# Performance work log

Hardware: AMD Instinct MI355X
Metric: run time of the kernel (lower is better)

## Reference

```python
import jax, jax.numpy as jnp
from jax import lax
import numpy as np

B = 2048; IMG = 28; K = 3; CIN = 1; HC = 32; LC = 16; WID = 64; HID = 64
LIS = IMG - 3 * (K - 1)           # 22: latent image size
FLAT = LIS * LIS * HC             # 15488
BLK = WID * LC                    # 1024: hypernet block size
T1 = 10.0; T0 = 0.0; NSTEP = 20   # fixed-step RK4 replaces adaptive dopri5
VAR = 0.1                         # p_z0 diagonal covariance


def _conv(x, w, b):  # w: [Cout,Cin,k,k], VALID conv, stride 1
    y = lax.conv_general_dilated(x, w, (1, 1), 'VALID',
                                 dimension_numbers=('NCHW', 'OIHW', 'NCHW'))
    return y + b[None, :, None, None]


def _convT(x, w, b):  # w: [Cin,Cout,k,k] (pytorch ConvTranspose2d layout)
    wf = jnp.flip(w, (2, 3)).transpose(1, 0, 2, 3)  # -> OIHW, spatially flipped
    y = lax.conv_general_dilated(x, wf, (1, 1), [(K - 1, K - 1), (K - 1, K - 1)],
                                 dimension_numbers=('NCHW', 'OIHW', 'NCHW'))
    return y + b[None, :, None, None]


def _forward(x, c0w, c0b, c1w, c1b, c2w, c2b, elw, elb, dlw, dlb,
             t0w, t0b, t1w, t1b, t2w, t2b, h1w, h1b, h2w, h2b, h3w, h3b):
    # ---- encoder (dropout in eval = identity) ----
    h = jnp.tanh(_conv(x, c0w, c0b))
    h = jnp.tanh(_conv(h, c1w, c1b))
    h = jnp.tanh(_conv(h, c2w, c2b))
    z1 = h.reshape(h.shape[0], -1) @ elw + elb          # [B, LC]
    # ---- decoder ----
    d = jnp.tanh(z1 @ dlw + dlb)                         # [B, FLAT]
    d = d.reshape(-1, HC, LIS, LIS)
    d = jnp.tanh(_convT(d, t0w, t0b))
    d = jnp.tanh(_convT(d, t1w, t1b))
    recon = _convT(d, t2w, t2b)                          # [B, CIN, 28, 28]

    # ---- CNF vector field with analytic trace ----
    def hyper(t):
        p = jnp.tanh(jnp.reshape(jnp.asarray(t, jnp.float32), (1, 1)) @ h1w + h1b)
        p = jnp.tanh(p @ h2w + h2b)
        p = (p @ h3w + h3b).reshape(-1)
        W = p[:BLK].reshape(WID, LC)
        U = p[BLK:2 * BLK].reshape(WID, LC) * jax.nn.sigmoid(p[2 * BLK:3 * BLK].reshape(WID, LC))
        Bb = p[3 * BLK:]                                 # [WID]
        return W, Bb, U

    def f(t, z):
        W, Bb, U = hyper(t)
        hh = jnp.tanh(jnp.einsum('bd,wd->wb', z, W) + Bb[:, None])   # [WID, B]
        dz = jnp.einsum('wb,wd->bd', hh, U) / WID                     # [B, LC]
        s = jnp.sum(W * U, axis=1)                                    # [WID]: sum_i W_w[i]U_w[i]
        tr = jnp.mean((1.0 - hh * hh) * s[:, None], axis=0)           # [B] analytic trace
        return dz, -tr[:, None]

    dt = (T0 - T1) / NSTEP

    def step(state, i):
        z, lp = state
        t = T1 + i * dt
        k1z, k1l = f(t, z)
        k2z, k2l = f(t + 0.5 * dt, z + 0.5 * dt * k1z)
        k3z, k3l = f(t + 0.5 * dt, z + 0.5 * dt * k2z)
        k4z, k4l = f(t + dt, z + dt * k3z)
        z = z + dt / 6.0 * (k1z + 2 * k2z + 2 * k3z + k4z)
        lp = lp + dt / 6.0 * (k1l + 2 * k2l + 2 * k3l + k4l)
        return (z, lp), None

    lp1 = jnp.zeros((z1.shape[0], 1), z1.dtype)
    (z0, lp0), _ = lax.scan(step, (z1, lp1), jnp.arange(NSTEP, dtype=jnp.float32))

    # MultivariateNormal(0, 0.1*I) log_prob
    logp = -0.5 * (LC * jnp.log(2 * jnp.pi) + LC * jnp.log(VAR) + jnp.sum(z0 * z0, -1) / VAR)
    x_probs = jnp.mean(logp - lp0[:, 0])
    return recon, x_probs


def setup_inputs() -> dict:
    key = jax.random.key(0)
    ks = jax.random.split(key, 16)
    n = jax.random.normal
    s = jnp.float32(0.05)
    z = jnp.zeros
    OUT3 = 3 * BLK + WID
    return {
        'x': n(ks[0], (B, CIN, IMG, IMG), jnp.float32),
        'c0w': n(ks[1], (HC, CIN, K, K)) * s, 'c0b': z((HC,)),
        'c1w': n(ks[2], (HC, HC, K, K)) * s, 'c1b': z((HC,)),
        'c2w': n(ks[3], (HC, HC, K, K)) * s, 'c2b': z((HC,)),
        'elw': n(ks[4], (FLAT, LC)) * s, 'elb': z((LC,)),
        'dlw': n(ks[5], (LC, FLAT)) * s, 'dlb': z((FLAT,)),
        't0w': n(ks[6], (HC, HC, K, K)) * s, 't0b': z((HC,)),
        't1w': n(ks[7], (HC, HC, K, K)) * s, 't1b': z((HC,)),
        't2w': n(ks[8], (HC, CIN, K, K)) * s, 't2b': z((CIN,)),
        'h1w': n(ks[9], (1, HID)) * s, 'h1b': z((HID,)),
        'h2w': n(ks[10], (HID, HID)) * s, 'h2b': z((HID,)),
        'h3w': n(ks[11], (HID, OUT3)) * s, 'h3b': z((OUT3,)),
    }


def reference(x, c0w, c0b, c1w, c1b, c2w, c2b, elw, elb, dlw, dlb,
              t0w, t0b, t1w, t1b, t2w, t2b, h1w, h1b, h2w, h2b, h3w, h3b):
    return _forward(x, c0w, c0b, c1w, c1b, c2w, c2b, elw, elb, dlw, dlb,
                    t0w, t0b, t1w, t1b, t2w, t2b, h1w, h1b, h2w, h2b, h3w, h3b)
```

## Files before the change

kernel.cpp:

```cpp
#include <hip/hip_runtime.h>
#include <math.h>

#define Bsz 2048

using bf16x8 = __attribute__((ext_vector_type(8))) short;
using f32x4  = __attribute__((ext_vector_type(4))) float;

__device__ __forceinline__ float fast_tanh(float x){
    float e = __expf(2.0f * x);
    return 1.0f - 2.0f / (e + 1.0f);
}
__device__ __forceinline__ float fast_sigmoid(float x){
    return 1.0f / (1.0f + __expf(-x));
}
__device__ __forceinline__ unsigned short f2b(float f){
    union { float f; unsigned u; } v; v.f = f;
    unsigned r = v.u + 0x7FFFu + ((v.u >> 16) & 1u);
    return (unsigned short)(r >> 16);
}
__device__ __forceinline__ float b2f(unsigned short s){
    union { unsigned u; float f; } v; v.u = ((unsigned)s) << 16;
    return v.f;
}

__device__ __forceinline__ float stage_t(int sidx){
    int i  = sidx >> 2, st = sidx & 3;
    float t = 10.0f - 0.5f * (float)i;
    if (st == 1 || st == 2) t -= 0.25f;
    else if (st == 3)       t -= 0.5f;
    return t;
}

__global__ void k_prep(const float* __restrict__ c1w, const float* __restrict__ c2w,
                       const float* __restrict__ t0w, const float* __restrict__ t1w,
                       const float* __restrict__ elw, const float* __restrict__ dlw,
                       const float* __restrict__ elb,
                       unsigned short* __restrict__ wc1, unsigned short* __restrict__ wc2,
                       unsigned short* __restrict__ wt0, unsigned short* __restrict__ wt1,
                       unsigned short* __restrict__ elwT, unsigned short* __restrict__ dlwT,
                       float* __restrict__ z1, int full){
    int gsz = gridDim.x * 256;
    for (int i = blockIdx.x*256 + threadIdx.x; i < 9216; i += gsz){
        int ci = i & 31, co = (i >> 5) & 31, s = i >> 10;
        wc1[i] = f2b(c1w[(co*32 + ci)*9 + s]);
        wc2[i] = f2b(c2w[(co*32 + ci)*9 + s]);
        wt0[i] = f2b(t0w[(ci*32 + co)*9 + (8 - s)]);
        wt1[i] = f2b(t1w[(ci*32 + co)*9 + (8 - s)]);
    }
    if (!full) return;
    for (int i = blockIdx.x*256 + threadIdx.x; i < 32768; i += gsz)
        z1[i] = elb[i & 15];
    for (int i = blockIdx.x*256 + threadIdx.x; i < 247808; i += gsz){
        int l = i / 15488, f2 = i - l*15488;
        int pos = f2 >> 5, ci = f2 & 31;
        elwT[i] = f2b(elw[(ci*484 + pos)*16 + l]);
    }
    for (int i = blockIdx.x*256 + threadIdx.x; i < 247808; i += gsz){
        int f2 = i >> 4, l = i & 15;
        int pos = f2 >> 5, ci = f2 & 31;
        dlwT[i] = f2b(dlw[l*15488 + ci*484 + pos]);
    }
}

__global__ void __launch_bounds__(256)
k_conv0(const float* __restrict__ x, const float* __restrict__ c0w,
        const float* __restrict__ c0b, unsigned short* __restrict__ A0,
        int cb, int CH){
    int gid = blockIdx.x*256 + threadIdx.x;
    if (gid >= CH*676) return;
    int b = gid / 676, pos = gid - b*676;
    int y = pos / 26, xx = pos - y*26;
    const float* xin = x + (size_t)(cb + b)*784;
    float v[9];
#pragma unroll
    for (int r = 0; r < 3; r++)
#pragma unroll
        for (int s = 0; s < 3; s++)
            v[r*3+s] = xin[(y+r)*28 + xx + s];
    unsigned short* ob = A0 + (size_t)b*21632 + pos*32;
#pragma unroll
    for (int g = 0; g < 8; g++){
        float a0 = c0b[g*4+0], a1 = c0b[g*4+1], a2 = c0b[g*4+2], a3 = c0b[g*4+3];
#pragma unroll
        for (int k = 0; k < 9; k++){
            a0 += v[k] * c0w[(g*4+0)*9 + k];
            a1 += v[k] * c0w[(g*4+1)*9 + k];
            a2 += v[k] * c0w[(g*4+2)*9 + k];
            a3 += v[k] * c0w[(g*4+3)*9 + k];
        }
        ushort4 o;
        o.x = f2b(fast_tanh(a0)); o.y = f2b(fast_tanh(a1));
        o.z = f2b(fast_tanh(a2)); o.w = f2b(fast_tanh(a3));
        *(ushort4*)(ob + g*4) = o;
    }
}

template<int IL, int OL, int OW, int OOFF, int INS, int OUTS>
__global__ void __launch_bounds__(256)
k_convM(const unsigned short* __restrict__ in, const unsigned short* __restrict__ wg,
        const float* __restrict__ bias, unsigned short* __restrict__ out, int CH){
    constexpr int N  = OL * OL;
    constexpr int NT = (N + 15) / 16;
    const int tid = threadIdx.x;
    const int wave = tid >> 6, lane = tid & 63;
    const int q = lane >> 4, nn = lane & 15;
    const int nw = gridDim.x * 4;

    bf16x8 af[2][9];
#pragma unroll
    for (int mt = 0; mt < 2; mt++)
#pragma unroll
        for (int s = 0; s < 9; s++)
            af[mt][s] = *(const bf16x8*)(wg + s*1024 + (mt*16 + nn)*32 + q*8);
    float4 bc0 = *(const float4*)(bias + q*4);
    float4 bc1 = *(const float4*)(bias + 16 + q*4);

    for (int t = blockIdx.x*4 + wave; t < CH*NT; t += nw){
        int img = t / NT, tt = t - img*NT;
        const unsigned short* inb = in + (size_t)img * INS;
        unsigned short* outb = out + (size_t)img * OUTS;
        int pos = tt*16 + nn;
        int pc  = pos < N ? pos : N - 1;
        int oy = pc / OL, ox = pc - oy*OL;
        const unsigned short* ib = inb + (oy*IL + ox)*32 + q*8;
        f32x4 acc0 = {0.f,0.f,0.f,0.f}, acc1 = {0.f,0.f,0.f,0.f};
#pragma unroll
        for (int r = 0; r < 3; r++){
            bf16x8 b0 = *(const bf16x8*)(ib + (r*IL + 0)*32);
            bf16x8 b1 = *(const bf16x8*)(ib + (r*IL + 1)*32);
            bf16x8 b2 = *(const bf16x8*)(ib + (r*IL + 2)*32);
            acc0 = __builtin_amdgcn_mfma_f32_16x16x32_bf16(af[0][r*3+0], b0, acc0, 0,0,0);
            acc1 = __builtin_amdgcn_mfma_f32_16x16x32_bf16(af[1][r*3+0], b0, acc1, 0,0,0);
            acc0 = __builtin_amdgcn_mfma_f32_16x16x32_bf16(af[0][r*3+1], b1, acc0, 0,0,0);
            acc1 = __builtin_amdgcn_mfma_f32_16x16x32_bf16(af[1][r*3+1], b1, acc1, 0,0,0);
            acc0 = __builtin_amdgcn_mfma_f32_16x16x32_bf16(af[0][r*3+2], b2, acc0, 0,0,0);
            acc1 = __builtin_amdgcn_mfma_f32_16x16x32_bf16(af[1][r*3+2], b2, acc1, 0,0,0);
        }
        if (pos < N){
            int opix = oy*OW + ox + OOFF;
            ushort4 o0, o1;
            o0.x = f2b(fast_tanh(acc0[0] + bc0.x)); o0.y = f2b(fast_tanh(acc0[1] + bc0.y));
            o0.z = f2b(fast_tanh(acc0[2] + bc0.z)); o0.w = f2b(fast_tanh(acc0[3] + bc0.w));
            o1.x = f2b(fast_tanh(acc1[0] + bc1.x)); o1.y = f2b(fast_tanh(acc1[1] + bc1.y));
            o1.z = f2b(fast_tanh(acc1[2] + bc1.z)); o1.w = f2b(fast_tanh(acc1[3] + bc1.w));
            *(ushort4*)(outb + opix*32 + q*4)      = o0;
            *(ushort4*)(outb + opix*32 + 16 + q*4) = o1;
        }
    }
}

__global__ void __launch_bounds__(256)
k_encg(const unsigned short* __restrict__ A2, const unsigned short* __restrict__ elwT,
       float* __restrict__ z1, int cb, int CH){
    int wave = threadIdx.x >> 6, lane = threadIdx.x & 63;
    int q = lane >> 4, nn = lane & 15;
    int imgb = blockIdx.x*16;
    const unsigned short* ap = A2 + (size_t)(imgb + nn)*21632 + q*8;
    const unsigned short* bp = elwT + (size_t)nn*15488 + q*8;
    f32x4 acc = {0.f,0.f,0.f,0.f};
    int s0 = blockIdx.y*121;
#pragma unroll 2
    for (int s = s0 + wave; s < s0 + 121; s += 4){
        bf16x8 a = *(const bf16x8*)(ap + s*32);
        bf16x8 b = *(const bf16x8*)(bp + s*32);
        acc = __builtin_amdgcn_mfma_f32_16x16x32_bf16(a, b, acc, 0,0,0);
    }
    float* zp = z1 + (size_t)(cb + imgb)*16;
#pragma unroll
    for (int i = 0; i < 4; i++)
        atomicAdd(zp + (q*4 + i)*16 + nn, acc[i]);
}

__global__ void __launch_bounds__(256)
k_decg(const float* __restrict__ z1, const unsigned short* __restrict__ dlwT,
       const float* __restrict__ dlb, unsigned short* __restrict__ D0,
       unsigned short* __restrict__ D1, int cb, int CH){
    __shared__ float zl[256];
    int tid = threadIdx.x, ib = blockIdx.y;
    zl[tid] = z1[(size_t)(cb + ib*16 + (tid >> 4))*16 + (tid & 15)];
    __syncthreads();
    if (blockIdx.x >= 61){
        int hid = (blockIdx.x - 61)*256 + tid;
        uint4 zq = {0,0,0,0};
        for (int p = hid; p < 16*676; p += 1280){
            int im = p / 676, px = p - im*676;
            int y = px / 26, x = px - y*26;
            if (y < 2 || y >= 24 || x < 2 || x >= 24){
                uint4* pt = (uint4*)(D0 + (size_t)(ib*16 + im)*21632 + px*32);
                pt[0] = zq; pt[1] = zq; pt[2] = zq; pt[3] = zq;
            }
        }
        for (int p = hid; p < 16*784; p += 1280){
            int im = p / 784, px = p - im*784;
            int y = px / 28, x = px - y*28;
            if (y < 2 || y >= 26 || x < 2 || x >= 26){
                uint4* pt = (uint4*)(D1 + (size_t)(ib*16 + im)*25088 + px*32);
                pt[0] = zq; pt[1] = zq; pt[2] = zq; pt[3] = zq;
            }
        }
        return;
    }
    int ci = tid & 31, po = tid >> 5;
    int pos = blockIdx.x*8 + po;
    if (pos >= 484) return;
    int y = pos / 22, xx = pos - y*22;
    float bias = dlb[ci*484 + pos];
    const unsigned short* w = dlwT + (size_t)(pos*32 + ci)*16;
    bf16x8 w0 = *(const bf16x8*)(w);
    bf16x8 w1 = *(const bf16x8*)(w + 8);
    float wf[16];
#pragma unroll
    for (int j = 0; j < 8; j++){
        wf[j]   = b2f((unsigned short)w0[j]);
        wf[8+j] = b2f((unsigned short)w1[j]);
    }
    int opix = ((y+2)*26 + xx + 2)*32 + ci;
#pragma unroll 1
    for (int i = 0; i < 16; i++){
        float a = bias;
#pragma unroll
        for (int l = 0; l < 16; l++) a += zl[i*16 + l] * wf[l];
        D0[(size_t)(ib*16 + i)*21632 + opix] = f2b(fast_tanh(a));
    }
}

__global__ void __launch_bounds__(256)
k_convT2(const unsigned short* __restrict__ D2, const float* __restrict__ t2w,
         const float* __restrict__ t2b, float* __restrict__ out, int cb, int CH){
    int gid = blockIdx.x*256 + threadIdx.x;
    if (gid >= CH*784) return;
    int b = gid / 784, o = gid - b*784;
    int y = o / 28, xx = o - y*28;
    const unsigned short* db = D2 + (size_t)b*21632;
    float a = t2b[0];
#pragma unroll
    for (int r = 0; r < 3; r++){
        int iy = y + r - 2;
        if ((unsigned)iy >= 26u) continue;
#pragma unroll
        for (int s = 0; s < 3; s++){
            int ix = xx + s - 2;
            if ((unsigned)ix >= 26u) continue;
            const unsigned short* pp = db + (iy*26 + ix)*32;
            int wi = (2-r)*3 + (2-s);
#pragma unroll
            for (int g = 0; g < 4; g++){
                bf16x8 h = *(const bf16x8*)(pp + g*8);
#pragma unroll
                for (int j = 0; j < 8; j++)
                    a += b2f((unsigned short)h[j]) * t2w[(g*8+j)*9 + wi];
            }
        }
    }
    out[(size_t)(cb + b)*784 + o] = a;
}

template<int LOUT, int INW, int OUTW, int OUTOFF>
__device__ __forceinline__ void conv_gemm(const unsigned short* __restrict__ Wg,
                                          const float* __restrict__ bias,
                                          const unsigned short* inL,
                                          unsigned short* outL, int tid){
    constexpr int N  = LOUT * LOUT;
    constexpr int NT = (N + 15) / 16;
    const int lane  = tid & 63;
    const int wave  = tid >> 6;
    const int mtile = wave & 1;
    const int quad  = lane >> 4;
    const int nn    = lane & 15;
    bf16x8 afr[9];
    const unsigned short* wp = Wg + (mtile*16 + nn)*32 + quad*8;
#pragma unroll
    for (int s = 0; s < 9; s++)
        afr[s] = *(const bf16x8*)(wp + s*1024);
    float4 bco = *(const float4*)(bias + mtile*16 + quad*4);
    for (int t = (wave >> 1); t < NT; t += 2){
        int pos = t*16 + nn;
        int pc  = pos < N ? pos : N - 1;
        int y = pc / LOUT, x = pc - y*LOUT;
        const unsigned short* ib = inL + (y*INW + x)*32 + quad*8;
        f32x4 acc = {0.f, 0.f, 0.f, 0.f};
#pragma unroll
        for (int r = 0; r < 3; r++)
#pragma unroll
            for (int s = 0; s < 3; s++)
                acc = __builtin_amdgcn_mfma_f32_16x16x32_bf16(
                        afr[r*3+s], *(const bf16x8*)(ib + (r*INW + s)*32), acc, 0, 0, 0);
        if (pos < N){
            ushort4 o;
            o.x = f2b(fast_tanh(acc[0] + bco.x));
            o.y = f2b(fast_tanh(acc[1] + bco.y));
            o.z = f2b(fast_tanh(acc[2] + bco.z));
            o.w = f2b(fast_tanh(acc[3] + bco.w));
            int opix = y*OUTW + x + OUTOFF;
            *(ushort4*)(outL + opix*32 + mtile*16 + quad*4) = o;
        }
    }
}

__global__ void __launch_bounds__(256)
k_enc_f(const float* __restrict__ x,
        const float* __restrict__ c0w, const float* __restrict__ c0b,
        const unsigned short* __restrict__ wc1, const float* __restrict__ c1b,
        const unsigned short* __restrict__ wc2, const float* __restrict__ c2b,
        const float* __restrict__ elw, const float* __restrict__ elb,
        float* __restrict__ z1){
    __shared__ float X[784];
    __shared__ __align__(16) unsigned short H0[21632];
    __shared__ __align__(16) unsigned short H1[18432];
    __shared__ __align__(16) unsigned short H2[15488];
    __shared__ float red[16*17];
    const int tid = threadIdx.x, b = blockIdx.x;
    for (int i = tid; i < 784; i += 256) X[i] = x[b*784 + i];
    __syncthreads();
    for (int pos = tid; pos < 676; pos += 256){
        int y = pos / 26, xx = pos - y*26;
        float v[9];
#pragma unroll
        for (int r = 0; r < 3; r++)
#pragma unroll
            for (int s = 0; s < 3; s++)
                v[r*3+s] = X[(y+r)*28 + xx + s];
#pragma unroll
        for (int g = 0; g < 8; g++){
            float a0 = c0b[g*4+0], a1 = c0b[g*4+1], a2 = c0b[g*4+2], a3 = c0b[g*4+3];
#pragma unroll
            for (int k = 0; k < 9; k++){
                a0 += v[k] * c0w[(g*4+0)*9 + k];
                a1 += v[k] * c0w[(g*4+1)*9 + k];
                a2 += v[k] * c0w[(g*4+2)*9 + k];
                a3 += v[k] * c0w[(g*4+3)*9 + k];
            }
            ushort4 o;
            o.x = f2b(fast_tanh(a0)); o.y = f2b(fast_tanh(a1));
            o.z = f2b(fast_tanh(a2)); o.w = f2b(fast_tanh(a3));
            *(ushort4*)(H0 + pos*32 + g*4) = o;
        }
    }
    __syncthreads();
    conv_gemm<24, 26, 24, 0>(wc1, c1b, H0, H1, tid);
    __syncthreads();
    conv_gemm<22, 24, 22, 0>(wc2, c2b, H1, H2, tid);
    __syncthreads();
    {
        int fg = tid >> 4, l = tid & 15;
        float a = 0.f;
        for (int ci = 0; ci < 32; ci++)
            for (int pos = fg; pos < 484; pos += 16)
                a += b2f(H2[pos*32 + ci]) * elw[(ci*484 + pos)*16 + l];
        red[fg*17 + l] = a;
        __syncthreads();
        if (tid < 16){
            float s = elb[tid];
#pragma unroll
            for (int g = 0; g < 16; g++) s += red[g*17 + tid];
            z1[b*16 + tid] = s;
        }
    }
}

__global__ void __launch_bounds__(256)
k_dec_f(const float* __restrict__ z1,
        const float* __restrict__ dlw, const float* __restrict__ dlb,
        const unsigned short* __restrict__ wt0, const float* __restrict__ t0b,
        const unsigned short* __restrict__ wt1, const float* __restrict__ t1b,
        const float* __restrict__ t2w, const float* __restrict__ t2b,
        float* __restrict__ out){
    __shared__ __align__(16) unsigned short D0[21632];
    __shared__ __align__(16) unsigned short D1[25088];
    __shared__ __align__(16) unsigned short D2[28800];
    const int tid = threadIdx.x, b = blockIdx.x;
    {
        uint4 zq = {0,0,0,0};
        for (int i = tid; i < 2704; i += 256) ((uint4*)D0)[i] = zq;
        for (int i = tid; i < 3136; i += 256) ((uint4*)D1)[i] = zq;
        for (int i = tid; i < 3600; i += 256) ((uint4*)D2)[i] = zq;
    }
    float zz[16];
#pragma unroll
    for (int l = 0; l < 16; l++) zz[l] = z1[b*16 + l];
    __syncthreads();
    for (int f = tid; f < 15488; f += 256){
        float a = dlb[f];
#pragma unroll
        for (int l = 0; l < 16; l++) a += zz[l] * dlw[l*15488 + f];
        int ci = f / 484, pos = f - ci*484;
        int y = pos / 22, xx = pos - y*22;
        D0[((y+2)*26 + xx + 2)*32 + ci] = f2b(fast_tanh(a));
    }
    __syncthreads();
    conv_gemm<24, 26, 28, 58>(wt0, t0b, D0, D1, tid);
    __syncthreads();
    conv_gemm<26, 28, 30, 62>(wt1, t1b, D1, D2, tid);
    __syncthreads();
    for (int o = tid; o < 784; o += 256){
        int y = o / 28, xx = o - y*28;
        float a = t2b[0];
#pragma unroll
        for (int r = 0; r < 3; r++)
#pragma unroll
            for (int s = 0; s < 3; s++){
                const unsigned short* pp = D2 + ((y+r)*30 + xx + s)*32;
                int wi = (2-r)*3 + (2-s);
#pragma unroll
                for (int g = 0; g < 4; g++){
                    bf16x8 h = *(const bf16x8*)(pp + g*8);
#pragma unroll
                    for (int j = 0; j < 8; j++)
                        a += b2f((unsigned short)h[j]) * t2w[(g*8+j)*9 + wi];
                }
            }
        out[(size_t)b*784 + o] = a;
    }
}

__global__ void __launch_bounds__(64)
k_hyp1(const float* __restrict__ h1w, const float* __restrict__ h1b,
       const float* __restrict__ h2w, const float* __restrict__ h2b,
       float* __restrict__ p2ws){
    __shared__ float p1l[64];
    int sidx = blockIdx.x, tid = threadIdx.x;
    float t = stage_t(sidx);
    p1l[tid] = fast_tanh(t * h1w[tid] + h1b[tid]);
    __syncthreads();
    float a0 = h2b[tid], a1 = 0.f, a2 = 0.f, a3 = 0.f;
#pragma unroll
    for (int k = 0; k < 64; k += 4){
        a0 += p1l[k]   * h2w[(k)*64   + tid];
        a1 += p1l[k+1] * h2w[(k+1)*64 + tid];
        a2 += p1l[k+2] * h2w[(k+2)*64 + tid];
        a3 += p1l[k+3] * h2w[(k+3)*64 + tid];
    }
    p2ws[sidx*64 + tid] = fast_tanh((a0 + a1) + (a2 + a3));
}

__global__ void __launch_bounds__(256)
k_hyp2(const float* __restrict__ p2ws, const float* __restrict__ h3w,
       const float* __restrict__ h3b, float* __restrict__ p3ws){
    __shared__ float p2l[64];
    int sidx = blockIdx.y, tid = threadIdx.x;
    if (tid < 64) p2l[tid] = p2ws[sidx*64 + tid];
    __syncthreads();
    int m = blockIdx.x*256 + tid;
    if (m >= 3136) return;
    const float* hp = h3w + m;
    float a0 = h3b[m], a1 = 0.f, a2 = 0.f, a3 = 0.f;
#pragma unroll
    for (int k = 0; k < 64; k += 4){
        a0 += p2l[k]   * hp[(size_t)(k)*3136];
        a1 += p2l[k+1] * hp[(size_t)(k+1)*3136];
        a2 += p2l[k+2] * hp[(size_t)(k+2)*3136];
        a3 += p2l[k+3] * hp[(size_t)(k+3)*3136];
    }
    p3ws[(size_t)sidx*3200 + m] = (a0 + a1) + (a2 + a3);
}

__global__ void __launch_bounds__(256)
k_hyp3(const float* __restrict__ p3ws, float* __restrict__ hyp){
    __shared__ float sred[64];
    int sidx = blockIdx.x, tid = threadIdx.x;
    const float* p3 = p3ws + (size_t)sidx*3200;
    float* g = hyp + (size_t)sidx*2048;
    unsigned short* gW = (unsigned short*)g;
    unsigned short* gU = (unsigned short*)(g + 1024);

    {
        int lane = tid & 63, c = tid >> 6;
        int q = lane >> 4, m = lane & 15;
        ushort4 o0 = {0,0,0,0}, o1 = {0,0,0,0};
        if (q < 2){
            const float* wp = p3 + (c*16 + m)*16 + q*8;
            o0.x = f2b(wp[0]); o0.y = f2b(wp[1]); o0.z = f2b(wp[2]); o0.w = f2b(wp[3]);
            o1.x = f2b(wp[4]); o1.y = f2b(wp[5]); o1.z = f2b(wp[6]); o1.w = f2b(wp[7]);
        }
        *(ushort4*)(gW + tid*8)     = o0;
        *(ushort4*)(gW + tid*8 + 4) = o1;
    }
    if (tid < 128){
        int lane = tid & 63, kb = tid >> 6;
        int q = lane >> 4, d = lane & 15;
        unsigned short uo[8];
#pragma unroll
        for (int j = 0; j < 8; j++){
            int w = kb*32 + q*8 + j;
            float u = p3[1024 + w*16 + d] * fast_sigmoid(p3[2048 + w*16 + d]);
            uo[j] = f2b(u);
        }
        *(ushort4*)(gU + tid*8)     = *(ushort4*)&uo[0];
        *(ushort4*)(gU + tid*8 + 4) = *(ushort4*)&uo[4];
    } else if (tid < 192){
        int w = tid - 128;
        g[1536 + w] = p3[3072 + w];
    } else {
        int w = tid - 192;
        float s = 0.f;
#pragma unroll
        for (int d = 0; d < 16; d++){
            float u = p3[1024 + w*16 + d] * fast_sigmoid(p3[2048 + w*16 + d]);
            s += p3[w*16 + d] * u;
        }
        g[1600 + w] = s;
        sred[w] = s;
    }
    __syncthreads();
    if (tid == 0){
        float st = 0.f;
#pragma unroll
        for (int w = 0; w < 64; w++) st += sred[w];
        g[1664] = st;
    }
}

__global__ void k_hyper(const float* __restrict__ h1w, const float* __restrict__ h1b,
                        const float* __restrict__ h2w, const float* __restrict__ h2b,
                        const float* __restrict__ h3w, const float* __restrict__ h3b,
                        float* __restrict__ hyp){
    int sidx = blockIdx.x;
    float t = stage_t(sidx);
    __shared__ float p1[64], p2[64];
    __shared__ float p3[3136];
    int tid = threadIdx.x;
    if (tid < 64) p1[tid] = fast_tanh(t * h1w[tid] + h1b[tid]);
    __syncthreads();
    if (tid < 64){
        float a = h2b[tid];
#pragma unroll
        for (int k = 0; k < 64; k++) a += p1[k] * h2w[k*64 + tid];
        p2[tid] = fast_tanh(a);
    }
    __syncthreads();
    for (int m = tid; m < 3136; m += 256){
        float a = h3b[m];
#pragma unroll
        for (int k = 0; k < 64; k++) a += p2[k] * h3w[k*3136 + m];
        p3[m] = a;
    }
    __syncthreads();
    float* g = hyp + (size_t)sidx * 2304;
    for (int m = tid; m < 1024; m += 256){
        g[m] = p3[m];
        float u = p3[1024 + m] * fast_sigmoid(p3[2048 + m]);
        g[1024 + (m & 15)*64 + (m >> 4)] = u;
        p3[1024 + m] = u;
    }
    if (tid < 64) g[2048 + tid] = p3[3072 + tid];
    __syncthreads();
    if (tid < 64){
        float s = 0.f;
#pragma unroll
        for (int d = 0; d < 16; d++) s += p3[tid*16 + d] * p3[1024 + tid*16 + d];
        g[2112 + tid] = s;
    }
}

struct PM {
    bf16x8 Wf[4];
    bf16x8 Uf[2];
    float4 Bbf[4];
    float4 sf[4];
    float stot;
};
__device__ __forceinline__ void loadPM(const float* __restrict__ g, int lane, int q, PM& p){
    const unsigned short* gW = (const unsigned short*)g;
    const unsigned short* gU = (const unsigned short*)(g + 1024);
#pragma unroll
    for (int c = 0; c < 4; c++)
        p.Wf[c] = *(const bf16x8*)(gW + (c*64 + lane)*8);
#pragma unroll
    for (int kb = 0; kb < 2; kb++)
        p.Uf[kb] = *(const bf16x8*)(gU + (kb*64 + lane)*8);
#pragma unroll
    for (int c = 0; c < 4; c++){
        p.Bbf[c] = *(const float4*)(g + 1536 + c*16 + q*4);
        p.sf[c]  = *(const float4*)(g + 1600 + c*16 + q*4);
    }
    p.stot = g[1664];
}

__global__ void __launch_bounds__(64)
k_cnfM(const float* __restrict__ z1, const float* __restrict__ hyp,
       float* __restrict__ part){
    __shared__ __align__(16) unsigned short zsb[16*24];
    __shared__ __align__(16) unsigned short hhT[16*72];
    const int lane = threadIdx.x;
    const int q = lane >> 4, d = lane & 15;
    const float dt = -0.5f;

    float z[4], zacc[4], lacc[4], lp[4];
#pragma unroll
    for (int i = 0; i < 4; i++){
        z[i] = z1[(size_t)(blockIdx.x*16 + q*4 + i)*16 + d];
        zacc[i] = 0.f; lacc[i] = 0.f; lp[i] = 0.f;
        zsb[(q*4 + i)*24 + d] = f2b(z[i]);
    }
    PM pm0, pm1;
    loadPM(hyp, lane, q, pm0);

#pragma unroll 2
    for (int sidx = 0; sidx < 80; sidx++){
        PM& cur = (sidx & 1) ? pm1 : pm0;
        PM& nxt = (sidx & 1) ? pm0 : pm1;
        if (sidx < 79) loadPM(hyp + (size_t)(sidx + 1)*2048, lane, q, nxt);

        bf16x8 zb;
        if (q < 2) zb = *(const bf16x8*)(zsb + d*24 + q*8);
        else { bf16x8 zz2 = {0,0,0,0,0,0,0,0}; zb = zz2; }

        f32x4 h0 = {0,0,0,0}, h1 = {0,0,0,0}, h2 = {0,0,0,0}, h3 = {0,0,0,0};
        h0 = __builtin_amdgcn_mfma_f32_16x16x32_bf16(cur.Wf[0], zb, h0, 0,0,0);
        h1 = __builtin_amdgcn_mfma_f32_16x16x32_bf16(cur.Wf[1], zb, h1, 0,0,0);
        h2 = __builtin_amdgcn_mfma_f32_16x16x32_bf16(cur.Wf[2], zb, h2, 0,0,0);
        h3 = __builtin_amdgcn_mfma_f32_16x16x32_bf16(cur.Wf[3], zb, h3, 0,0,0);

        float partial = 0.f;
        f32x4 hc[4] = {h0, h1, h2, h3};
#pragma unroll
        for (int c = 0; c < 4; c++){
            ushort4 o;
// ... 28 lines not shown
            if (st < 3){
                float aa = (st == 2) ? 1.0f : 0.5f;
                zsv = z[i] + aa * dt * dz;
            } else {
                z[i]  += (dt/6.f) * zacc[i];
                lp[i] += (dt/6.f) * lacc[i];
                zsv = z[i];
                zacc[i] = 0.f; lacc[i] = 0.f;
            }
            zsb[(q*4 + i)*24 + d] = f2b(zsv);
        }
    }
    float sq[4];
#pragma unroll
    for (int i = 0; i < 4; i++) sq[i] = z[i]*z[i];
#pragma unroll
    for (int off = 1; off < 16; off <<= 1){
#pragma unroll
        for (int i = 0; i < 4; i++) sq[i] += __shfl_xor(sq[i], off, 16);
    }
    if (d == 0){
#pragma unroll
        for (int i = 0; i < 4; i++){
            float logp = -0.5f * (16.f*1.8378770664093453f
                                 + 16.f*(-2.302585092994046f) + sq[i]*10.f);
            part[blockIdx.x*16 + q*4 + i] = logp - lp[i];
        }
    }
}

struct PF { float4 Wr[4]; float4 Ur[4]; float Bb, sw; };
__device__ __forceinline__ void load_pf(const float* __restrict__ g,
                                        int lane, int q, int d, PF& p){
    const float4* w4 = (const float4*)(g + lane*16);
    p.Wr[0] = w4[0]; p.Wr[1] = w4[1]; p.Wr[2] = w4[2]; p.Wr[3] = w4[3];
    const float4* u4 = (const float4*)(g + 1024 + d*64 + q*16);
    p.Ur[0] = u4[0]; p.Ur[1] = u4[1]; p.Ur[2] = u4[2]; p.Ur[3] = u4[3];
    p.Bb = g[2048 + lane];
    p.sw = g[2112 + lane];
}
__global__ void __launch_bounds__(64)
k_cnf_f(const float* __restrict__ z1, const float* __restrict__ hyp,
        float* __restrict__ part){
    __shared__ __align__(16) float zsl[16];
    __shared__ __align__(16) float hhl[64];
    const int lane = threadIdx.x;
    const int q = lane >> 4, d = lane & 15;
    const float dt = -0.5f;
    float z  = z1[(size_t)blockIdx.x*16 + d];
    float zs = z;
    float lp = 0.f, zacc = 0.f, lacc = 0.f;
    if (lane < 16) zsl[lane] = zs;
    PF cur, nxt;
    load_pf(hyp, lane, q, d, cur);
    for (int sidx = 0; sidx < 80; sidx++){
        __syncthreads();
        if (sidx < 79) load_pf(hyp + (size_t)(sidx + 1)*2304, lane, q, d, nxt);
        const float4* zp = (const float4*)zsl;
        float4 z0 = zp[0], z1v = zp[1], z2 = zp[2], z3 = zp[3];
        float a = cur.Bb;
        a += z0.x*cur.Wr[0].x + z0.y*cur.Wr[0].y + z0.z*cur.Wr[0].z + z0.w*cur.Wr[0].w;
        a += z1v.x*cur.Wr[1].x + z1v.y*cur.Wr[1].y + z1v.z*cur.Wr[1].z + z1v.w*cur.Wr[1].w;
        a += z2.x*cur.Wr[2].x + z2.y*cur.Wr[2].y + z2.z*cur.Wr[2].z + z2.w*cur.Wr[2].w;
        a += z3.x*cur.Wr[3].x + z3.y*cur.Wr[3].y + z3.z*cur.Wr[3].z + z3.w*cur.Wr[3].w;
        float hh = fast_tanh(a);
        float e = (1.f - hh*hh) * cur.sw;
#pragma unroll
        for (int off = 1; off < 64; off <<= 1)
            e += __shfl_xor(e, off);
        hhl[lane] = hh;
        __syncthreads();
        const float4* hp = (const float4*)(hhl + q*16);
        float4 h0 = hp[0], h1 = hp[1], h2 = hp[2], h3 = hp[3];
        float dzp = 0.f;
        dzp += h0.x*cur.Ur[0].x + h0.y*cur.Ur[0].y + h0.z*cur.Ur[0].z + h0.w*cur.Ur[0].w;
        dzp += h1.x*cur.Ur[1].x + h1.y*cur.Ur[1].y + h1.z*cur.Ur[1].z + h1.w*cur.Ur[1].w;
        dzp += h2.x*cur.Ur[2].x + h2.y*cur.Ur[2].y + h2.z*cur.Ur[2].z + h2.w*cur.Ur[2].w;
        dzp += h3.x*cur.Ur[3].x + h3.y*cur.Ur[3].y + h3.z*cur.Ur[3].z + h3.w*cur.Ur[3].w;
        dzp += __shfl_xor(dzp, 16);
        dzp += __shfl_xor(dzp, 32);
        float dz = dzp * (1.f/64.f);
        float dl = -e  * (1.f/64.f);
        int st = sidx & 3;
        float wgt = (st == 0 || st == 3) ? 1.f : 2.f;
        zacc += wgt * dz;
        lacc += wgt * dl;
        if (st < 3){
            float aa = (st == 2) ? 1.0f : 0.5f;
            zs = z + aa * dt * dz;
        } else {
            z  += (dt/6.f) * zacc;
            lp += (dt/6.f) * lacc;
            zs = z;
            zacc = 0.f; lacc = 0.f;
        }
        if (lane < 16) zsl[lane] = zs;
        cur = nxt;
    }
    float sq = z * z;
#pragma unroll
    for (int off = 1; off < 16; off <<= 1) sq += __shfl_xor(sq, off, 16);
    float logp = -0.5f * (16.f*1.8378770664093453f + 16.f*(-2.302585092994046f) + sq*10.f);
    if (lane == 0) part[blockIdx.x] = logp - lp;
}

__global__ void k_final(const float* __restrict__ part, float* __restrict__ out){
    __shared__ float red[256];
    int tid = threadIdx.x;
    float s = 0.f;
#pragma unroll
    for (int k = 0; k < 8; k++) s += part[tid + k*256];
    red[tid] = s;
    __syncthreads();
    for (int st = 128; st > 0; st >>= 1){
        if (tid < st) red[tid] += red[tid + st];
        __syncthreads();
    }
    if (tid == 0) out[1605632] = red[0] * (1.f/2048.f);
}

extern "C" void kernel_launch(void* const* d_in, const int* in_sizes, int n_in,
                              void* d_out, int out_size, void* d_ws, size_t ws_size,
                              hipStream_t stream){
    const float* x   = (const float*)d_in[0];
    const float* c0w = (const float*)d_in[1];
    const float* c0b = (const float*)d_in[2];
    const float* c1w = (const float*)d_in[3];
    const float* c1b = (const float*)d_in[4];
    const float* c2w = (const float*)d_in[5];
    const float* c2b = (const float*)d_in[6];
    const float* elw = (const float*)d_in[7];
    const float* elb = (const float*)d_in[8];
    const float* dlw = (const float*)d_in[9];
    const float* dlb = (const float*)d_in[10];
    const float* t0w = (const float*)d_in[11];
    const float* t0b = (const float*)d_in[12];
    const float* t1w = (const float*)d_in[13];
    const float* t1b = (const float*)d_in[14];
    const float* t2w = (const float*)d_in[15];
    const float* t2b = (const float*)d_in[16];
    const float* h1w = (const float*)d_in[17];
    const float* h1b = (const float*)d_in[18];
    const float* h2w = (const float*)d_in[19];
    const float* h2b = (const float*)d_in[20];
    const float* h3w = (const float*)d_in[21];
    const float* h3b = (const float*)d_in[22];

    float* ws   = (float*)d_ws;
    float* z1   = ws;
    float* hyp  = z1 + 32768;
    float* part = hyp + 184320;
    float* p2ws = part + 2048;
    float* p3ws = p2ws + 5120;
    unsigned short* wc1  = (unsigned short*)(p3ws + 256000);
    unsigned short* wc2  = wc1 + 9216;
    unsigned short* wt0  = wc2 + 9216;
    unsigned short* wt1  = wt0 + 9216;
    unsigned short* elwT = wt1 + 9216;
    unsigned short* dlwT = elwT + 247808;
    unsigned short* act  = dlwT + 247808;
    float* rec  = (float*)d_out;

    const size_t MISC = 2985984;
    int CH = 0;
    const int cands[6] = {2048, 1024, 512, 256, 128, 64};
    for (int c = 0; c < 6; c++){
        size_t need = MISC + (size_t)cands[c] * 93440;
        if (need <= ws_size){ CH = cands[c]; break; }
    }

    if (CH == 0){
        k_hyper<<<80, 256, 0, stream>>>(h1w, h1b, h2w, h2b, h3w, h3b, hyp);
        k_prep <<<64,   256, 0, stream>>>(c1w, c2w, t0w, t1w, elw, dlw, elb,
                                          wc1, wc2, wt0, wt1, wt1, wt1, z1, 0);
        k_enc_f<<<2048, 256, 0, stream>>>(x, c0w, c0b, wc1, c1b, wc2, c2b, elw, elb, z1);
        k_cnf_f<<<2048,  64, 0, stream>>>(z1, hyp, part);
        k_dec_f<<<2048, 256, 0, stream>>>(z1, dlw, dlb, wt0, t0b, wt1, t1b, t2w, t2b, rec);
        k_final<<<1,    256, 0, stream>>>(part, rec);
        return;
    }

    k_hyp1<<<80,           64, 0, stream>>>(h1w, h1b, h2w, h2b, p2ws);
    k_hyp2<<<dim3(13,80), 256, 0, stream>>>(p2ws, h3w, h3b, p3ws);
    k_hyp3<<<80,          256, 0, stream>>>(p3ws, hyp);

    k_prep<<<64, 256, 0, stream>>>(c1w, c2w, t0w, t1w, elw, dlw, elb,
                                   wc1, wc2, wt0, wt1, elwT, dlwT, z1, 1);

    unsigned short* Y = act;
    unsigned short* X = Y + (size_t)CH*21632;

    for (int cb = 0; cb < Bsz; cb += CH){
        k_conv0<<<(CH*676 + 255)/256, 256, 0, stream>>>(x, c0w, c0b, Y, cb, CH);
        k_convM<26,24,24, 0, 21632, 25088><<<(CH*36 + 15)/16, 256, 0, stream>>>(Y, wc1, c1b, X, CH);
        k_convM<24,22,22, 0, 25088, 21632><<<(CH*31 + 15)/16, 256, 0, stream>>>(X, wc2, c2b, Y, CH);
        k_encg<<<dim3(CH/16, 4), 256, 0, stream>>>(Y, elwT, z1, cb, CH);
        k_decg<<<dim3(66, CH/16), 256, 0, stream>>>(z1, dlwT, dlb, Y, X, cb, CH);
        k_convM<26,24,28,58, 21632, 25088><<<(CH*36 + 15)/16, 256, 0, stream>>>(Y, wt0, t0b, X, CH);
        k_convM<28,26,26, 0, 25088, 21632><<<(CH*43 + 15)/16, 256, 0, stream>>>(X, wt1, t1b, Y, CH);
        k_convT2<<<(CH*784 + 255)/256, 256, 0, stream>>>(Y, t2w, t2b, rec, cb, CH);
    }
    k_cnfM <<<128,  64, 0, stream>>>(z1, hyp, part);
    k_final<<<1,   256, 0, stream>>>(part, rec);
}
```

Measured before the change: 636.5 us.

## Fuse conv layers pairwise per image through LDS to cut activation traffic

The encoder's first conv is merged with the second conv in one kernel per image, with conv0's output kept in padded shared memory. The decoder linear layer is fused with the first transposed conv, and the second transposed conv with the final one, both through shared memory. This removes several global round trips of bf16 activations and some kernel launches, and shrinks the per-chunk workspace. The cost is one block per image with about 54KB of LDS, which limits occupancy, and a serial prologue phase inside each block.

Measured after the change: 653.8 us. +2.7%, slower.

```diff
diff --git a/kernel.cpp b/kernel.cpp
--- a/kernel.cpp
+++ b/kernel.cpp
@@ -34,11 +34,11 @@
 __global__ void k_prep(const float* __restrict__ c1w, const float* __restrict__ c2w,
                        const float* __restrict__ t0w, const float* __restrict__ t1w,
                        const float* __restrict__ elw, const float* __restrict__ dlw,
-                       const float* __restrict__ elb,
+                       const float* __restrict__ elb, const float* __restrict__ dlb,
                        unsigned short* __restrict__ wc1, unsigned short* __restrict__ wc2,
                        unsigned short* __restrict__ wt0, unsigned short* __restrict__ wt1,
                        unsigned short* __restrict__ elwT, unsigned short* __restrict__ dlwT,
-                       float* __restrict__ z1, int full){
+                       float* __restrict__ dlbT, float* __restrict__ z1, int full){
     int gsz = gridDim.x * 256;
     for (int i = blockIdx.x*256 + threadIdx.x; i < 9216; i += gsz){
         int ci = i & 31, co = (i >> 5) & 31, s = i >> 10;
@@ -50,6 +50,10 @@
     if (!full) return;
     for (int i = blockIdx.x*256 + threadIdx.x; i < 32768; i += gsz)
         z1[i] = elb[i & 15];
+    for (int i = blockIdx.x*256 + threadIdx.x; i < 15488; i += gsz){
+        int pos = i >> 5, ci = i & 31;
+        dlbT[i] = dlb[ci*484 + pos];
+    }
     for (int i = blockIdx.x*256 + threadIdx.x; i < 247808; i += gsz){
         int l = i / 15488, f2 = i - l*15488;
         int pos = f2 >> 5, ci = f2 & 31;
@@ -63,35 +67,78 @@
 }
 
 __global__ void __launch_bounds__(256)
-k_conv0(const float* __restrict__ x, const float* __restrict__ c0w,
-        const float* __restrict__ c0b, unsigned short* __restrict__ A0,
-        int cb, int CH){
-    int gid = blockIdx.x*256 + threadIdx.x;
-    if (gid >= CH*676) return;
-    int b = gid / 676, pos = gid - b*676;
-    int y = pos / 26, xx = pos - y*26;
+k_enc01(const float* __restrict__ x, const float* __restrict__ c0w,
+        const float* __restrict__ c0b, const unsigned short* __restrict__ wc1,
+        const float* __restrict__ c1b, unsigned short* __restrict__ A1,
+        int cb){
+    __shared__ __align__(16) unsigned short A0L[676*40];
+    const int tid = threadIdx.x, b = blockIdx.x;
     const float* xin = x + (size_t)(cb + b)*784;
-    float v[9];
-#pragma unroll
-    for (int r = 0; r < 3; r++)
-#pragma unroll
-        for (int s = 0; s < 3; s++)
-            v[r*3+s] = xin[(y+r)*28 + xx + s];
-    unsigned short* ob = A0 + (size_t)b*21632 + pos*32;
-#pragma unroll
-    for (int g = 0; g < 8; g++){
-        float a0 = c0b[g*4+0], a1 = c0b[g*4+1], a2 = c0b[g*4+2], a3 = c0b[g*4+3];
-#pragma unroll
-        for (int k = 0; k < 9; k++){
-            a0 += v[k] * c0w[(g*4+0)*9 + k];
-            a1 += v[k] * c0w[(g*4+1)*9 + k];
-            a2 += v[k] * c0w[(g*4+2)*9 + k];
-            a3 += v[k] * c0w[(g*4+3)*9 + k];
-        }
-        ushort4 o;
-        o.x = f2b(fast_tanh(a0)); o.y = f2b(fast_tanh(a1));
-        o.z = f2b(fast_tanh(a2)); o.w = f2b(fast_tanh(a3));
-        *(ushort4*)(ob + g*4) = o;
+
+    for (int pos = tid; pos < 676; pos += 256){
+        int y = pos / 26, xx = pos - y*26;
+        float v[9];
+#pragma unroll
+        for (int r = 0; r < 3; r++)
+#pragma unroll
+            for (int s = 0; s < 3; s++)
+                v[r*3+s] = xin[(y+r)*28 + xx + s];
+        unsigned short* ob = A0L + pos*40;
+#pragma unroll
+        for (int g = 0; g < 8; g++){
+            float a0 = c0b[g*4+0], a1 = c0b[g*4+1], a2 = c0b[g*4+2], a3 = c0b[g*4+3];
+#pragma unroll
+            for (int k = 0; k < 9; k++){
+                a0 += v[k] * c0w[(g*4+0)*9 + k];
+                a1 += v[k] * c0w[(g*4+1)*9 + k];
+                a2 += v[k] * c0w[(g*4+2)*9 + k];
+                a3 += v[k] * c0w[(g*4+3)*9 + k];
+            }
+            ushort4 o;
+            o.x = f2b(fast_tanh(a0)); o.y = f2b(fast_tanh(a1));
+            o.z = f2b(fast_tanh(a2)); o.w = f2b(fast_tanh(a3));
+            *(ushort4*)(ob + g*4) = o;
+        }
+    }
+    __syncthreads();
+
+    const int wave = tid >> 6, lane = tid & 63;
+    const int q = lane >> 4, nn = lane & 15;
+    bf16x8 af[2][9];
+#pragma unroll
+    for (int mt = 0; mt < 2; mt++)
+#pragma unroll
+        for (int s = 0; s < 9; s++)
+            af[mt][s] = *(const bf16x8*)(wc1 + s*1024 + (mt*16 + nn)*32 + q*8);
+    float4 bc0 = *(const float4*)(c1b + q*4);
+    float4 bc1 = *(const float4*)(c1b + 16 + q*4);
+    unsigned short* outb = A1 + (size_t)b*25088;
+
+    for (int t = wave; t < 36; t += 4){
+        int pos = t*16 + nn;
+        int oy = pos / 24, ox = pos - oy*24;
+        const unsigned short* ib = A0L + (oy*26 + ox)*40 + q*8;
+        f32x4 acc0 = {0.f,0.f,0.f,0.f}, acc1 = {0.f,0.f,0.f,0.f};
+#pragma unroll
+        for (int r = 0; r < 3; r++){
+            bf16x8 b0 = *(const bf16x8*)(ib + (r*26 + 0)*40);
+            bf16x8 b1 = *(const bf16x8*)(ib + (r*26 + 1)*40);
+            bf16x8 b2 = *(const bf16x8*)(ib + (r*26 + 2)*40);
+            acc0 = __builtin_amdgcn_mfma_f32_16x16x32_bf16(af[0][r*3+0], b0, acc0, 0,0,0);
+            acc1 = __builtin_amdgcn_mfma_f32_16x16x32_bf16(af[1][r*3+0], b0, acc1, 0,0,0);
+            acc0 = __builtin_amdgcn_mfma_f32_16x16x32_bf16(af[0][r*3+1], b1, acc0, 0,0,0);
+            acc1 = __builtin_amdgcn_mfma_f32_16x16x32_bf16(af[1][r*3+1], b1, acc1, 0,0,0);
+            acc0 = __builtin_amdgcn_mfma_f32_16x16x32_bf16(af[0][r*3+2], b2, acc0, 0,0,0);
+            acc1 = __builtin_amdgcn_mfma_f32_16x16x32_bf16(af[1][r*3+2], b2, acc1, 0,0,0);
+        }
+        int opix = oy*24 + ox;
+        ushort4 o0, o1;
+        o0.x = f2b(fast_tanh(acc0[0] + bc0.x)); o0.y = f2b(fast_tanh(acc0[1] + bc0.y));
+        o0.z = f2b(fast_tanh(acc0[2] + bc0.z)); o0.w = f2b(fast_tanh(acc0[3] + bc0.w));
+        o1.x = f2b(fast_tanh(acc1[0] + bc1.x)); o1.y = f2b(fast_tanh(acc1[1] + bc1.y));
+        o1.z = f2b(fast_tanh(acc1[2] + bc1.z)); o1.w = f2b(fast_tanh(acc1[3] + bc1.w));
+        *(ushort4*)(outb + opix*32 + q*4)      = o0;
+        *(ushort4*)(outb + opix*32 + 16 + q*4) = o1;
     }
 }
 
@@ -155,7 +202,7 @@
     int wave = threadIdx.x >> 6, lane = threadIdx.x & 63;
     int q = lane >> 4, nn = lane & 15;
     int imgb = blockIdx.x*16;
-    const unsigned short* ap = A2 + (size_t)(imgb + nn)*21632 + q*8;
+    const unsigned short* ap = A2 + (size_t)(imgb + nn)*15488 + q*8;
     const unsigned short* bp = elwT + (size_t)nn*15488 + q*8;
     f32x4 acc = {0.f,0.f,0.f,0.f};
     int s0 = blockIdx.y*121;
@@ -172,87 +219,168 @@
 }
 
 __global__ void __launch_bounds__(256)
-k_decg(const float* __restrict__ z1, const unsigned short* __restrict__ dlwT,
-       const float* __restrict__ dlb, unsigned short* __restrict__ D0,
-       unsigned short* __restrict__ D1, int cb, int CH){
-    __shared__ float zl[256];
-    int tid = threadIdx.x, ib = blockIdx.y;
-    zl[tid] = z1[(size_t)(cb + ib*16 + (tid >> 4))*16 + (tid & 15)];
-    __syncthreads();
-    if (blockIdx.x >= 61){
-        int hid = (blockIdx.x - 61)*256 + tid;
+k_dect0(const float* __restrict__ z1, const unsigned short* __restrict__ dlwT,
+        const float* __restrict__ dlbT, const unsigned short* __restrict__ wt0,
+        const float* __restrict__ t0b, unsigned short* __restrict__ D1, int cb){
+    __shared__ __align__(16) unsigned short D0L[676*40];
+    const int tid = threadIdx.x, b = blockIdx.x;
+    unsigned short* d1b = D1 + (size_t)b*25088;
+
+    {
         uint4 zq = {0,0,0,0};
-        for (int p = hid; p < 16*676; p += 1280){
-            int im = p / 676, px = p - im*676;
-            int y = px / 26, x = px - y*26;
-            if (y < 2 || y >= 24 || x < 2 || x >= 24){
-                uint4* pt = (uint4*)(D0 + (size_t)(ib*16 + im)*21632 + px*32);
+        for (int p = tid; p < 676; p += 256){
+            int y = p / 26, xx = p - y*26;
+            if (y < 2 || y >= 24 || xx < 2 || xx >= 24){
+                uint4* pt = (uint4*)(D0L + p*40);
                 pt[0] = zq; pt[1] = zq; pt[2] = zq; pt[3] = zq;
             }
         }
-        for (int p = hid; p < 16*784; p += 1280){
-            int im = p / 784, px = p - im*784;
-            int y = px / 28, x = px - y*28;
-            if (y < 2 || y >= 26 || x < 2 || x >= 26){
-                uint4* pt = (uint4*)(D1 + (size_t)(ib*16 + im)*25088 + px*32);
+        for (int p = tid; p < 784; p += 256){
+            int y = p / 28, xx = p - y*28;
+            if (y < 2 || y >= 26 || xx < 2 || xx >= 26){
+                uint4* pt = (uint4*)(d1b + p*32);
                 pt[0] = zq; pt[1] = zq; pt[2] = zq; pt[3] = zq;
             }
         }
-        return;
-    }
-    int ci = tid & 31, po = tid >> 5;
-    int pos = blockIdx.x*8 + po;
-    if (pos >= 484) return;
-    int y = pos / 22, xx = pos - y*22;
-    float bias = dlb[ci*484 + pos];
-    const unsigned short* w = dlwT + (size_t)(pos*32 + ci)*16;
-    bf16x8 w0 = *(const bf16x8*)(w);
-    bf16x8 w1 = *(const bf16x8*)(w + 8);
-    float wf[16];
-#pragma unroll
-    for (int j = 0; j < 8; j++){
-        wf[j]   = b2f((unsigned short)w0[j]);
-        wf[8+j] = b2f((unsigned short)w1[j]);
-    }
-    int opix = ((y+2)*26 + xx + 2)*32 + ci;
-#pragma unroll 1
-    for (int i = 0; i < 16; i++){
-        float a = bias;
-#pragma unroll
-        for (int l = 0; l < 16; l++) a += zl[i*16 + l] * wf[l];
-        D0[(size_t)(ib*16 + i)*21632 + opix] = f2b(fast_tanh(a));
+    }
+    float zz[16];
+#pragma unroll
+    for (int l = 0; l < 16; l++) zz[l] = z1[(size_t)(cb + b)*16 + l];
+    {
+        int ci = tid & 31, po = tid >> 5;
+#pragma unroll 2
+        for (int rr = 0; rr < 61; rr++){
+            int pos = rr*8 + po;
+            if (pos < 484){
+                int y = pos / 22, xx = pos - y*22;
+                const unsigned short* w = dlwT + (size_t)(pos*32 + ci)*16;
+                bf16x8 w0 = *(const bf16x8*)(w);
+                bf16x8 w1 = *(const bf16x8*)(w + 8);
+                float a = dlbT[pos*32 + ci];
+#pragma unroll
+                for (int j = 0; j < 8; j++){
+                    a += zz[j]     * b2f((unsigned short)w0[j]);
+                    a += zz[8 + j] * b2f((unsigned short)w1[j]);
+                }
+                D0L[((y+2)*26 + xx + 2)*40 + ci] = f2b(fast_tanh(a));
+            }
+        }
+    }
+    __syncthreads();
+
+    const int wave = tid >> 6, lane = tid & 63;
+    const int q = lane >> 4, nn = lane & 15;
+    bf16x8 af[2][9];
+#pragma unroll
+    for (int mt = 0; mt < 2; mt++)
+#pragma unroll
+        for (int s = 0; s < 9; s++)
+            af[mt][s] = *(const bf16x8*)(wt0 + s*1024 + (mt*16 + nn)*32 + q*8);
+    float4 bc0 = *(const float4*)(t0b + q*4);
+    float4 bc1 = *(const float4*)(t0b + 16 + q*4);
+
+    for (int t = wave; t < 36; t += 4){
+        int pos = t*16 + nn;
+        int oy = pos / 24, ox = pos - oy*24;
+        const unsigned short* ib = D0L + (oy*26 + ox)*40 + q*8;
+        f32x4 acc0 = {0.f,0.f,0.f,0.f}, acc1 = {0.f,0.f,0.f,0.f};
+#pragma unroll
+        for (int r = 0; r < 3; r++){
+            bf16x8 b0 = *(const bf16x8*)(ib + (r*26 + 0)*40);
+            bf16x8 b1 = *(const bf16x8*)(ib + (r*26 + 1)*40);
+            bf16x8 b2 = *(const bf16x8*)(ib + (r*26 + 2)*40);
+            acc0 = __builtin_amdgcn_mfma_f32_16x16x32_bf16(af[0][r*3+0], b0, acc0, 0,0,0);
+            acc1 = __builtin_amdgcn_mfma_f32_16x16x32_bf16(af[1][r*3+0], b0, acc1, 0,0,0);
+            acc0 = __builtin_amdgcn_mfma_f32_16x16x32_bf16(af[0][r*3+1], b1, acc0, 0,0,0);
+            acc1 = __builtin_amdgcn_mfma_f32_16x16x32_bf16(af[1][r*3+1], b1, acc1, 0,0,0);
+            acc0 = __builtin_amdgcn_mfma_f32_16x16x32_bf16(af[0][r*3+2], b2, acc0, 0,0,0);
+            acc1 = __builtin_amdgcn_mfma_f32_16x16x32_bf16(af[1][r*3+2], b2, acc1, 0,0,0);
+        }
+        int opix = oy*28 + ox + 58;
+        ushort4 o0, o1;
+        o0.x = f2b(fast_tanh(acc0[0] + bc0.x)); o0.y = f2b(fast_tanh(acc0[1] + bc0.y));
+        o0.z = f2b(fast_tanh(acc0[2] + bc0.z)); o0.w = f2b(fast_tanh(acc0[3] + bc0.w));
+        o1.x = f2b(fast_tanh(acc1[0] + bc1.x)); o1.y = f2b(fast_tanh(acc1[1] + bc1.y));
+        o1.z = f2b(fast_tanh(acc1[2] + bc1.z)); o1.w = f2b(fast_tanh(acc1[3] + bc1.w));
+        *(ushort4*)(d1b + opix*32 + q*4)      = o0;
+        *(ushort4*)(d1b + opix*32 + 16 + q*4) = o1;
     }
 }
 
 __global__ void __launch_bounds__(256)
-k_convT2(const unsigned short* __restrict__ D2, const float* __restrict__ t2w,
-         const float* __restrict__ t2b, float* __restrict__ out, int cb, int CH){
-    int gid = blockIdx.x*256 + threadIdx.x;
-    if (gid >= CH*784) return;
-    int b = gid / 784, o = gid - b*784;
-    int y = o / 28, xx = o - y*28;
-    const unsigned short* db = D2 + (size_t)b*21632;
-    float a = t2b[0];
-#pragma unroll
-    for (int r = 0; r < 3; r++){
-        int iy = y + r - 2;
-        if ((unsigned)iy >= 26u) continue;
-#pragma unroll
-        for (int s = 0; s < 3; s++){
-            int ix = xx + s - 2;
-            if ((unsigned)ix >= 26u) continue;
-            const unsigned short* pp = db + (iy*26 + ix)*32;
-            int wi = (2-r)*3 + (2-s);
-#pragma unroll
-            for (int g = 0; g < 4; g++){
-                bf16x8 h = *(const bf16x8*)(pp + g*8);
-#pragma unroll
-                for (int j = 0; j < 8; j++)
-                    a += b2f((unsigned short)h[j]) * t2w[(g*8+j)*9 + wi];
+k_dect12(const unsigned short* __restrict__ D1, const unsigned short* __restrict__ wt1,
+         const float* __restrict__ t1b, const float* __restrict__ t2w,
+         const float* __restrict__ t2b, float* __restrict__ out, int cb){
+    __shared__ __align__(16) unsigned short D2L[676*40];
+    const int tid = threadIdx.x, b = blockIdx.x;
+    const unsigned short* d1b = D1 + (size_t)b*25088;
+    const int wave = tid >> 6, lane = tid & 63;
+    const int q = lane >> 4, nn = lane & 15;
+
+    bf16x8 af[2][9];
+#pragma unroll
+    for (int mt = 0; mt < 2; mt++)
+#pragma unroll
+        for (int s = 0; s < 9; s++)
+            af[mt][s] = *(const bf16x8*)(wt1 + s*1024 + (mt*16 + nn)*32 + q*8);
+    float4 bc0 = *(const float4*)(t1b + q*4);
+    float4 bc1 = *(const float4*)(t1b + 16 + q*4);
+
+    for (int t = wave; t < 43; t += 4){
+        int pos = t*16 + nn;
+        int pc  = pos < 676 ? pos : 675;
+        int oy = pc / 26, ox = pc - oy*26;
+        const unsigned short* ib = d1b + (oy*28 + ox)*32 + q*8;
+        f32x4 acc0 = {0.f,0.f,0.f,0.f}, acc1 = {0.f,0.f,0.f,0.f};
+#pragma unroll
+        for (int r = 0; r < 3; r++){
+            bf16x8 b0 = *(const bf16x8*)(ib + (r*28 + 0)*32);
+            bf16x8 b1 = *(const bf16x8*)(ib + (r*28 + 1)*32);
+            bf16x8 b2 = *(const bf16x8*)(ib + (r*28 + 2)*32);
+            acc0 = __builtin_amdgcn_mfma_f32_16x16x32_bf16(af[0][r*3+0], b0, acc0, 0,0,0);
+            acc1 = __builtin_amdgcn_mfma_f32_16x16x32_bf16(af[1][r*3+0], b0, acc1, 0,0,0);
+            acc0 = __builtin_amdgcn_mfma_f32_16x16x32_bf16(af[0][r*3+1], b1, acc0, 0,0,0);
+            acc1 = __builtin_amdgcn_mfma_f32_16x16x32_bf16(af[1][r*3+1], b1, acc1, 0,0,0);
+            acc0 = __builtin_amdgcn_mfma_f32_16x16x32_bf16(af[0][r*3+2], b2, acc0, 0,0,0);
+            acc1 = __builtin_amdgcn_mfma_f32_16x16x32_bf16(af[1][r*3+2], b2, acc1, 0,0,0);
+        }
+        if (pos < 676){
+            int opix = oy*26 + ox;
+            ushort4 o0, o1;
+            o0.x = f2b(fast_tanh(acc0[0] + bc0.x)); o0.y = f2b(fast_tanh(acc0[1] + bc0.y));
+            o0.z = f2b(fast_tanh(acc0[2] + bc0.z)); o0.w = f2b(fast_tanh(acc0[3] + bc0.w));
+            o1.x = f2b(fast_tanh(acc1[0] + bc1.x)); o1.y = f2b(fast_tanh(acc1[1] + bc1.y));
+            o1.z = f2b(fast_tanh(acc1[2] + bc1.z)); o1.w = f2b(fast_tanh(acc1[3] + bc1.w));
+            *(ushort4*)(D2L + opix*40 + q*4)      = o0;
+            *(ushort4*)(D2L + opix*40 + 16 + q*4) = o1;
+        }
+    }
+    __syncthreads();
+
+    for (int o = tid; o < 784; o += 256){
+        int y = o / 28, xx = o - y*28;
+        float a = t2b[0];
+#pragma unroll
+        for (int r = 0; r < 3; r++){
+            int iy = y + r - 2;
+            if ((unsigned)iy >= 26u) continue;
+#pragma unroll
+            for (int s = 0; s < 3; s++){
+                int ix = xx + s - 2;
+                if ((unsigned)ix >= 26u) continue;
+                const unsigned short* pp = D2L + (iy*26 + ix)*40;
+                int wi = (2-r)*3 + (2-s);
+#pragma unroll
+                for (int g = 0; g < 4; g++){
+                    bf16x8 h = *(const bf16x8*)(pp + g*8);
+#pragma unroll
+                    for (int j = 0; j < 8; j++)
+                        a += b2f((unsigned short)h[j]) * t2w[(g*8+j)*9 + wi];
+                }
             }
         }
-    }
-    out[(size_t)(cb + b)*784 + o] = a;
+        out[(size_t)(cb + b)*784 + o] = a;
+    }
 }
 
 template<int LOUT, int INW, int OUTW, int OUTOFF>
@@ -462,7 +590,6 @@
     float* g = hyp + (size_t)sidx*2048;
     unsigned short* gW = (unsigned short*)g;
     unsigned short* gU = (unsigned short*)(g + 1024);
-
     {
         int lane = tid & 63, c = tid >> 6;
         int q = lane >> 4, m = lane & 15;
@@ -797,7 +924,8 @@
     float* part = hyp + 184320;
     float* p2ws = part + 2048;
     float* p3ws = p2ws + 5120;
-    unsigned short* wc1  = (unsigned short*)(p3ws + 256000);
+    float* dlbT = p3ws + 256000;
+    unsigned short* wc1  = (unsigned short*)(dlbT + 15488);
     unsigned short* wc2  = wc1 + 9216;
     unsigned short* wt0  = wc2 + 9216;
     unsigned short* wt1  = wt0 + 9216;
@@ -806,18 +934,18 @@
     unsigned short* act  = dlwT + 247808;
     float* rec  = (float*)d_out;
 
-    const size_t MISC = 2985984;
+    const size_t MISC = 3047936;
     int CH = 0;
     const int cands[6] = {2048, 1024, 512, 256, 128, 64};
     for (int c = 0; c < 6; c++){
-        size_t need = MISC + (size_t)cands[c] * 93440;
+        size_t need = MISC + (size_t)cands[c] * 81152;
         if (need <= ws_size){ CH = cands[c]; break; }
     }
 
     if (CH == 0){
         k_hyper<<<80, 256, 0, stream>>>(h1w, h1b, h2w, h2b, h3w, h3b, hyp);
-        k_prep <<<64,   256, 0, stream>>>(c1w, c2w, t0w, t1w, elw, dlw, elb,
-                                          wc1, wc2, wt0, wt1, wt1, wt1, z1, 0);
+        k_prep <<<64,   256, 0, stream>>>(c1w, c2w, t0w, t1w, elw, dlw, elb, dlb,
+                                          wc1, wc2, wt0, wt1, wt1, wt1, z1, z1, 0);
         k_enc_f<<<2048, 256, 0, stream>>>(x, c0w, c0b, wc1, c1b, wc2, c2b, elw, elb, z1);
         k_cnf_f<<<2048,  64, 0, stream>>>(z1, hyp, part);
         k_dec_f<<<2048, 256, 0, stream>>>(z1, dlw, dlb, wt0, t0b, wt1, t1b, t2w, t2b, rec);
@@ -829,21 +957,18 @@
     k_hyp2<<<dim3(13,80), 256, 0, stream>>>(p2ws, h3w, h3b, p3ws);
     k_hyp3<<<80,          256, 0, stream>>>(p3ws, hyp);
 
-    k_prep<<<64, 256, 0, stream>>>(c1w, c2w, t0w, t1w, elw, dlw, elb,
-                                   wc1, wc2, wt0, wt1, elwT, dlwT, z1, 1);
-
-    unsigned short* Y = act;
-    unsigned short* X = Y + (size_t)CH*21632;
+    k_prep<<<64, 256, 0, stream>>>(c1w, c2w, t0w, t1w, elw, dlw, elb, dlb,
+                                   wc1, wc2, wt0, wt1, elwT, dlwT, dlbT, z1, 1);
+
+    unsigned short* X = act;
+    unsigned short* Y = X + (size_t)CH*25088;
 
     for (int cb = 0; cb < Bsz; cb += CH){
-        k_conv0<<<(CH*676 + 255)/256, 256, 0, stream>>>(x, c0w, c0b, Y, cb, CH);
-        k_convM<26,24,24, 0, 21632, 25088><<<(CH*36 + 15)/16, 256, 0, stream>>>(Y, wc1, c1b, X, CH);
-        k_convM<24,22,22, 0, 25088, 21632><<<(CH*31 + 15)/16, 256, 0, stream>>>(X, wc2, c2b, Y, CH);
+        k_enc01<<<CH, 256, 0, stream>>>(x, c0w, c0b, wc1, c1b, X, cb);
+        k_convM<24,22,22,0, 25088, 15488><<<(CH*31 + 15)/16, 256, 0, stream>>>(X, wc2, c2b, Y, CH);
         k_encg<<<dim3(CH/16, 4), 256, 0, stream>>>(Y, elwT, z1, cb, CH);
-        k_decg<<<dim3(66, CH/16), 256, 0, stream>>>(z1, dlwT, dlb, Y, X, cb, CH);
-        k_convM<26,24,28,58, 21632, 25088><<<(CH*36 + 15)/16, 256, 0, stream>>>(Y, wt0, t0b, X, CH);
-        k_convM<28,26,26, 0, 25088, 21632><<<(CH*43 + 15)/16, 256, 0, stream>>>(X, wt1, t1b, Y, CH);
-        k_convT2<<<(CH*784 + 255)/256, 256, 0, stream>>>(Y, t2w, t2b, rec, cb, CH);
+        k_dect0<<<CH, 256, 0, stream>>>(z1, dlwT, dlbT, wt0, t0b, X, cb);
+        k_dect12<<<CH, 256, 0, stream>>>(X, wt1, t1b, t2w, t2b, rec, cb);
     }
     k_cnfM <<<128,  64, 0, stream>>>(z1, hyp, part);
     k_final<<<1,   256, 0, stream>>>(part, rec);
```
